# Optimization experiments

Measured on AMD Instinct MI355X. Metric: run time of the kernel, lower is better.

Reference implementation:

```python
import jax, jax.numpy as jnp
import numpy as np
import math

B, L = 16, 4096
N = B * L            # total nodes; node 0 is the (masked) root
E = N - 1            # one parent edge per non-root node
D_IN, D_OUT, HEADS = 512, 256, 4
SLOPE = 0.2          # PyG GATConv default negative_slope
PRUNE_FRAC = 0.3


def gelu(x):
    return 0.5 * x * (1.0 + jnp.tanh(math.sqrt(2.0 / math.pi) * (x + 0.044715 * x ** 3)))


def remove_nodes_func(parent, remove):
    # parent[i] = parent node id of node i+1; remove[j] = 1 iff node j+1 removed.
    for _ in range(5):
        aug_rem = jnp.concatenate([jnp.zeros(1, jnp.int32), remove])
        aug_par = jnp.concatenate([jnp.zeros(1, jnp.int32), parent])
        pr = aug_rem[parent]                               # is my parent removed?
        parent = pr * aug_par[parent] + (1 - pr) * parent  # grandparent if so
    return parent


def remove_nodes_and_edges(edge_index, map_index):
    src, par = edge_index[0], edge_index[1]
    rem = jnp.zeros(N, jnp.int32).at[map_index].set(1)     # removal flag per node id (>=1)
    edge_mask = 1 - rem[src]                               # drop edges whose child node removed
    emr = rem[1:]                                          # == zeros(E).at[map_index-1].set(1)
    temp = remove_nodes_func(par, emr)
    ei_new = jnp.stack([src, temp]) * edge_mask[None, :]   # removed edges collapse to (0,0)
    node_mask_upd = jnp.concatenate([jnp.ones(1, jnp.float32), 1.0 - emr.astype(jnp.float32)])
    return ei_new, node_mask_upd


def gat_conv(xin, edge_index, gat_w, att_src, att_dst, gat_b):
    # PyG GATConv: concat=True, add_self_loops=True, eval mode (attention dropout off)
    h = (xin @ gat_w).reshape(N, HEADS, D_OUT)
    loop = jnp.arange(N, dtype=edge_index.dtype)
    src = jnp.concatenate([edge_index[0], loop])
    dst = jnp.concatenate([edge_index[1], loop])
    a_src = jnp.einsum('nhc,hc->nh', h, att_src)
    a_dst = jnp.einsum('nhc,hc->nh', h, att_dst)
    alpha = jax.nn.leaky_relu(a_src[src] + a_dst[dst], SLOPE)       # [Etot, H]
    m = jax.ops.segment_max(alpha, dst, num_segments=N)
    e = jnp.exp(alpha - m[dst])
    s = jax.ops.segment_sum(e, dst, num_segments=N)
    coef = e / (s[dst] + 1e-16)
    out = jax.ops.segment_sum(coef[:, :, None] * h[src], dst, num_segments=N)
    return out.reshape(N, HEADS * D_OUT) + gat_b


def setup_inputs():
    key = jax.random.key(0)
    ks = jax.random.split(key, 10)
    x = jax.random.normal(ks[0], (N, D_IN), jnp.float32)
    statement_rep = jax.random.normal(ks[1], (N, D_IN), jnp.float32)
    node_mask = (jax.random.uniform(ks[2], (B, L)) > 0.3).astype(jnp.float32)
    node_mask = node_mask.at[0, 0].set(0.0)  # root node never scored/pruned
    type_id = jax.random.randint(ks[3], (B, L), 0, 2, dtype=jnp.int32)
    child = jnp.arange(1, N, dtype=jnp.int32)
    parent = jnp.floor(jax.random.uniform(ks[4], (E,)) * child).astype(jnp.int32)  # parent < child
    edge_index = jnp.stack([child, parent])
    edge_index_ent = edge_index
    s = 0.02
    scorer_w = jax.random.normal(ks[5], (2 * D_IN, 1), jnp.float32) * s
    scorer_b = jnp.zeros((1,), jnp.float32)
    emb_w = jax.random.normal(ks[6], (2, D_OUT), jnp.float32) * s
    emb_b = jnp.zeros((D_OUT,), jnp.float32)
    gat_w = jax.random.normal(ks[7], (2 * D_IN + D_OUT, HEADS * D_OUT), jnp.float32) * s
    att_src = jax.random.normal(ks[8], (HEADS, D_OUT), jnp.float32) * s
    att_dst = jax.random.normal(ks[9], (HEADS, D_OUT), jnp.float32) * s
    gat_b = jnp.zeros((HEADS * D_OUT,), jnp.float32)
    return {"x": x, "edge_index": edge_index, "edge_index_ent": edge_index_ent,
            "statement_rep": statement_rep, "node_mask": node_mask, "type_id": type_id,
            "scorer_w": scorer_w, "scorer_b": scorer_b, "emb_w": emb_w, "emb_b": emb_b,
            "gat_w": gat_w, "att_src": att_src, "att_dst": att_dst, "gat_b": gat_b}


def reference(x, edge_index, edge_index_ent, statement_rep, node_mask, type_id,
              scorer_w, scorer_b, emb_w, emb_b, gat_w, att_src, att_dst, gat_b):
    del edge_index_ent  # threaded through the original but never used
    nm = node_mask.reshape(-1)
    tid = type_id.reshape(-1)
    one_hot = jax.nn.one_hot(tid, 2, dtype=jnp.float32)
    type_emb = gelu(one_hot @ emb_w + emb_b)
    # --- single GNN layer (num_layers=1), with top-k node pruning ---
    node_score = (jnp.concatenate([x, statement_rep], 1) @ scorer_w + scorer_b)[:, 0] * nm
    nnz = int(jnp.count_nonzero(node_score))  # eager; k is data-dependent in the original
    if int(nnz * PRUNE_FRAC) != 0:
        k = int(nnz * PRUNE_FRAC + 1)
        masked = jnp.where(node_score != 0, node_score, jnp.inf)
        _, map_index = jax.lax.top_k(-masked, k)  # k smallest nonzero scores -> node ids
        edge_index, upd = remove_nodes_and_edges(edge_index, map_index)
        nm = nm * upd
    xin = jnp.concatenate([x, statement_rep, type_emb], 1)
    out = gelu(gat_conv(xin, edge_index, gat_w, att_src, att_dst, gat_b))
    # feature dropout runs in eval as identity here (deterministic reference)
    return out, nm.reshape(B, L)
```

## Files before the change

kernel.cpp:

```cpp
#include <hip/hip_runtime.h>
#include <cstdint>
#include <cstddef>

#define N_NODES 65536
#define E_EDGES 65535
#define DIN     512
#define KDIM    1024
#define JDIM    1024
#define HEADS   4
#define DOUT    256

typedef short   short8  __attribute__((ext_vector_type(8)));
typedef unsigned short ushort8 __attribute__((ext_vector_type(8)));
typedef float   floatx4 __attribute__((ext_vector_type(4)));

__device__ inline float bf2f(unsigned short u){
  union { unsigned int i; float f; } c; c.i = ((unsigned int)u) << 16; return c.f;
}
__device__ inline unsigned short f2bf(float f){
  union { float f; unsigned int i; } c; c.f = f;
  unsigned int r = c.i + 0x7FFFu + ((c.i >> 16) & 1u);
  return (unsigned short)(r >> 16);
}
__device__ inline unsigned int okey(float f){
  union { float f; unsigned int u; } c; c.f = f;
  return (c.u & 0x80000000u) ? ~c.u : (c.u | 0x80000000u);
}
__device__ inline float unokey(unsigned int k){
  union { unsigned int u; float f; } c;
  c.u = (k & 0x80000000u) ? (k ^ 0x80000000u) : ~k;
  return c.f;
}
__device__ inline float leaky(float x){ return x >= 0.f ? x : 0.2f * x; }
__device__ inline float gelu_f(float x){
  return 0.5f * x * (1.f + tanhf(0.7978845608028654f * (x + 0.044715f * x * x * x)));
}

__global__ void k_watt(const float* __restrict__ gw, const float* __restrict__ atts,
                       const float* __restrict__ attd, float* __restrict__ watt_s,
                       float* __restrict__ watt_d){
  int wave = threadIdx.x >> 6, lane = threadIdx.x & 63;
  int k = blockIdx.x*4 + wave;
  int hd = lane >> 4;
  const float* gr = gw + (size_t)k*JDIM + lane*16;
  float vs = 0.f, vd = 0.f;
  #pragma unroll
  for (int j = 0; j < 16; j += 4){
    float4 g = *(const float4*)(gr + j);
    float4 s = *(const float4*)(atts + lane*16 + j);
    float4 d = *(const float4*)(attd + lane*16 + j);
    vs += g.x*s.x + g.y*s.y + g.z*s.z + g.w*s.w;
    vd += g.x*d.x + g.y*d.y + g.z*d.z + g.w*d.w;
  }
  for (int m2 = 1; m2 < 16; m2 <<= 1){ vs += __shfl_xor(vs, m2); vd += __shfl_xor(vd, m2); }
  if ((lane & 15) == 0){ watt_s[k*4 + hd] = vs; watt_d[k*4 + hd] = vd; }
}

__global__ void k_tatt(const float* __restrict__ tc, const float* __restrict__ atts,
                       const float* __restrict__ attd, float* __restrict__ tatt){
  int lane = threadIdx.x;
  for (int o = 0; o < 16; o++){
    int ty = o >> 3, sd = (o >> 2) & 1, hd = o & 3;
    const float* av = sd ? attd : atts;
    float p = 0.f;
    #pragma unroll
    for (int cc = 0; cc < 4; cc++){
      int c = lane*4 + cc;
      p += tc[ty*JDIM + hd*256 + c] * av[hd*DOUT + c];
    }
    for (int sdel = 32; sdel; sdel >>= 1) p += __shfl_down(p, sdel);
    if (lane == 0) tatt[o] = p;
  }
}

__global__ void k_prep(const float* __restrict__ x, const float* __restrict__ sr,
                       const float* __restrict__ nmask, const float* __restrict__ sw,
                       const float* __restrict__ sb, const float* __restrict__ watt_s,
                       const float* __restrict__ watt_d, const float* __restrict__ tatt,
                       const int* __restrict__ tid, unsigned short* __restrict__ xs,
                       float* __restrict__ score, unsigned int* __restrict__ key,
                       float* __restrict__ asrc, float* __restrict__ adst){
  int lane = threadIdx.x & 63, wv = threadIdx.x >> 6;
  int i = blockIdx.x*4 + wv;
  const float* xr  = x  + (size_t)i*DIN;
  const float* srr = sr + (size_t)i*DIN;
  unsigned short* xo = xs + (size_t)i*KDIM;
  double part = 0.0;
  float4 ps = {0.f,0.f,0.f,0.f}, pd = {0.f,0.f,0.f,0.f};
  #pragma unroll
  for (int j = 0; j < 8; j++){
    int k = lane + 64*j;
    float va = xr[k];
    float vb = srr[k];
    part += (double)va*(double)sw[k] + (double)vb*(double)sw[512 + k];
    float4 sA = *(const float4*)(watt_s + (size_t)k*4);
    float4 dA = *(const float4*)(watt_d + (size_t)k*4);
    float4 sB = *(const float4*)(watt_s + (size_t)(512 + k)*4);
    float4 dB = *(const float4*)(watt_d + (size_t)(512 + k)*4);
    ps.x += va*sA.x + vb*sB.x; ps.y += va*sA.y + vb*sB.y;
    ps.z += va*sA.z + vb*sB.z; ps.w += va*sA.w + vb*sB.w;
    pd.x += va*dA.x + vb*dB.x; pd.y += va*dA.y + vb*dB.y;
    pd.z += va*dA.z + vb*dB.z; pd.w += va*dA.w + vb*dB.w;
    xo[k]       = f2bf(va);
    xo[512 + k] = f2bf(vb);
  }
  for (int sdel = 32; sdel; sdel >>= 1){
    part += __shfl_down(part, sdel);
    ps.x += __shfl_down(ps.x, sdel); ps.y += __shfl_down(ps.y, sdel);
    ps.z += __shfl_down(ps.z, sdel); ps.w += __shfl_down(ps.w, sdel);
    pd.x += __shfl_down(pd.x, sdel); pd.y += __shfl_down(pd.y, sdel);
    pd.z += __shfl_down(pd.z, sdel); pd.w += __shfl_down(pd.w, sdel);
  }
  if (lane == 0){
    float fs = (float)(part + (double)sb[0]);
    float s  = fs * nmask[i];
    score[i] = s;
    float v = (s == 0.f) ? __builtin_inff() : s;
    key[i] = okey(v);
    int tt = tid[i];
    float4 os = { ps.x + tatt[tt*8 + 0], ps.y + tatt[tt*8 + 1],
                  ps.z + tatt[tt*8 + 2], ps.w + tatt[tt*8 + 3] };
    float4 od = { pd.x + tatt[tt*8 + 4], pd.y + tatt[tt*8 + 5],
                  pd.z + tatt[tt*8 + 6], pd.w + tatt[tt*8 + 7] };
    *(float4*)(asrc + (size_t)i*HEADS) = os;
    *(float4*)(adst + (size_t)i*HEADS) = od;
  }
}

__global__ void k_nnz(const float* __restrict__ score, int* scal){
  int i = blockIdx.x*256 + threadIdx.x;
  int nz = (score[i] != 0.f) ? 1 : 0;
  unsigned long long b = __ballot(nz);
  if ((threadIdx.x & 63) == 0) atomicAdd(&scal[0], (int)__popcll(b));
}

__global__ void k_initsel(int* scal){
  int nnz = scal[0];
  double prod = (double)nnz * 0.3;
  scal[1] = ((int)prod != 0) ? 1 : 0;
  int k = (int)(prod + 1.0);
  scal[2] = k; scal[3] = 0; scal[4] = k;
}

__global__ void k_hist(const unsigned int* __restrict__ key, unsigned int* __restrict__ hist,
                       const int* __restrict__ scal, int pass){
  __shared__ unsigned int lh[256];
  int t = threadIdx.x;
  lh[t] = 0; __syncthreads();
  int i = blockIdx.x*256 + t;
  unsigned int kv = key[i];
  unsigned int pref = (unsigned int)scal[3];
  bool ok = (pass == 0) || ((kv >> (32 - 8*pass)) == pref);
  if (ok) atomicAdd(&lh[(kv >> (24 - 8*pass)) & 255u], 1u);
  __syncthreads();
  if (lh[t]) atomicAdd(&hist[t], lh[t]);
}

__global__ void k_select(unsigned int* __restrict__ hist, int* __restrict__ scal){
  __shared__ unsigned int h[256];
  int t = threadIdx.x;
  h[t] = hist[t];
  __syncthreads();
  if (t == 0){
    unsigned int r = (unsigned int)scal[4];
    unsigned int cum = 0, pref = (unsigned int)scal[3];
    for (int b = 0; b < 256; b++){
      unsigned int c = h[b];
      if (cum + c >= r){
        scal[3] = (int)((pref << 8) | (unsigned int)b);
        scal[4] = (int)(r - cum);
        break;
      }
      cum += c;
    }
  }
  __syncthreads();
  hist[t] = 0;
}

__global__ void k_mark(const unsigned int* __restrict__ key, int* __restrict__ scal,
                       int* __restrict__ rem, int* __restrict__ eqlist){
  if (!scal[1]) return;
  int i = blockIdx.x*256 + threadIdx.x;
  unsigned int Ks = (unsigned int)scal[3];
  unsigned int kv = key[i];
  if (kv < Ks) rem[i] = 1;
  else if (kv == Ks){
    int p = atomicAdd(&scal[5], 1);
    if (p < 4096) eqlist[p] = i;
  }
}

__global__ void k_ties(int* __restrict__ scal, int* __restrict__ eqlist, int* __restrict__ rem){
  if (!scal[1]) return;
  int m = scal[5]; if (m > 4096) m = 4096;
  int need = scal[4]; if (need > m) need = m;
  for (int it = 0; it < need; it++){
    int best = 0x7FFFFFFF, bj = -1;
    for (int j = 0; j < m; j++){ int v = eqlist[j]; if (v < best){ best = v; bj = j; } }
    if (bj < 0) break;
    rem[best] = 1; eqlist[bj] = 0x7FFFFFFF;
  }
}

__global__ void k_remap(const int* __restrict__ pin, const int* __restrict__ rem,
                        int* __restrict__ pout){
  int e = blockIdx.x*256 + threadIdx.x;
  if (e >= E_EDGES) return;
  int p = pin[e];
  pout[e] = rem[p] ? (p == 0 ? 0 : pin[p-1]) : p;
}

__global__ void k_edges(const int* __restrict__ srcIn, const int* __restrict__ pfin,
                        const int* __restrict__ rem, int* __restrict__ srcF,
                        int* __restrict__ dstF, int* __restrict__ cnt){
  int e = blockIdx.x*256 + threadIdx.x;
  if (e >= E_EDGES) return;
  int s = srcIn[e];
  if (rem[s]){ srcF[e] = 0; dstF[e] = -1; }
  else {
    srcF[e] = s;
    int d = pfin[e];
    dstF[e] = d;
    atomicAdd(&cnt[d], 1);
  }
}

__global__ void k_scan1(const int* __restrict__ cnt, int* __restrict__ offs,
                        int* __restrict__ bsum){
  int b = blockIdx.x, t = threadIdx.x, i = b*256 + t;
  int v = cnt[i];
  int lane = t & 63, wv = t >> 6;
  int xv = v;
  for (int o2 = 1; o2 < 64; o2 <<= 1){ int y = __shfl_up(xv, o2); if (lane >= o2) xv += y; }
  __shared__ int wt_[4];
  if (lane == 63) wt_[wv] = xv;
  __syncthreads();
  int add = 0;
  for (int k2 = 0; k2 < wv; k2++) add += wt_[k2];
  offs[i] = xv + add - v;
  if (t == 255) bsum[b] = xv + add;
}

__global__ void k_scan2(int* __restrict__ bsum){
  int t = threadIdx.x;
  int v = bsum[t];
  int lane = t & 63, wv = t >> 6;
  int xv = v;
  for (int o2 = 1; o2 < 64; o2 <<= 1){ int y = __shfl_up(xv, o2); if (lane >= o2) xv += y; }
  __shared__ int wt_[4];
  if (lane == 63) wt_[wv] = xv;
  __syncthreads();
  int add = 0;
  for (int k2 = 0; k2 < wv; k2++) add += wt_[k2];
  bsum[t] = xv + add - v;
}

__global__ void k_scan3(int* __restrict__ offs, const int* __restrict__ bsum,
                        int* __restrict__ cur){
  int b = blockIdx.x, t = threadIdx.x, i = b*256 + t;
  int v = offs[i] + bsum[b];
  offs[i] = v; cur[i] = v;
}

__global__ void k_fill(const int* __restrict__ dstF, int* __restrict__ cur,
                       int* __restrict__ elist){
  int e = blockIdx.x*256 + threadIdx.x;
  if (e >= E_EDGES) return;
  int d = dstF[e]; if (d < 0) return;
  int pos = atomicAdd(&cur[d], 1);
  elist[pos] = e;
}

__global__ void k_wt(const float* __restrict__ gw, unsigned short* __restrict__ wtb){
  __shared__ float tile[32][33];
  int kt = blockIdx.x*32, jt = blockIdx.y*32;
  int tx = threadIdx.x, ty = threadIdx.y;
  for (int r = ty; r < 32; r += 8) tile[r][tx] = gw[(size_t)(kt+r)*JDIM + jt + tx];
  __syncthreads();
  for (int r = ty; r < 32; r += 8) wtb[(size_t)(jt+r)*KDIM + kt + tx] = f2bf(tile[tx][r]);
}

__global__ void k_tc(const float* __restrict__ embw, const float* __restrict__ embb,
                     const float* __restrict__ gw, float* __restrict__ tc){
  __shared__ float eg[2][DOUT];
  int t = threadIdx.x;
  eg[0][t] = gelu_f(embw[t] + embb[t]);
  eg[1][t] = gelu_f(embw[DOUT + t] + embb[t]);
  __syncthreads();
  int g = blockIdx.x*256 + t;
  int te = g >> 10, j = g & 1023;
  float acc = 0.f;
  #pragma unroll 8
  for (int c = 0; c < DOUT; c++){
    acc += eg[te][c] * gw[(size_t)(KDIM + c)*JDIM + j];
  }
  tc[te*JDIM + j] = acc;
}

#define BKG 64
__global__ __launch_bounds__(512, 2) void k_gemm(const unsigned short* __restrict__ xs,
    const unsigned short* __restrict__ wtb, const float* __restrict__ tc,
    const int* __restrict__ tid, unsigned short* __restrict__ hmat){
  __shared__ unsigned short As[2][256*BKG];
  __shared__ unsigned short Bs[2][256*BKG];
  int bid = blockIdx.x;
  int xcd = bid & 7, tq = bid >> 3;
  int jb = tq & 3, ip = (tq >> 2)*8 + xcd;
  int rowbase = ip*256, colbase = jb*256;
  int t = threadIdx.x, wave = t >> 6, lane = t & 63;
  int wm = (wave >> 2)*128, wn = (wave & 3)*64;
  floatx4 acc[8][4];
  floatx4 zero = {0.f, 0.f, 0.f, 0.f};
  #pragma unroll
  for (int a = 0; a < 8; a++)
    #pragma unroll
    for (int b = 0; b < 4; b++) acc[a][b] = zero;

  int srow = lane >> 3;
  int scol = (lane & 7)*8;

  auto STAGE = [&](int buf, int kt){
    int k0 = kt*BKG;
    #pragma unroll
    for (int r = 0; r < 4; r++){
      int ci = r*8 + wave;
      int row = ci*8 + srow;
      const unsigned short* ga = xs  + (size_t)(rowbase + row)*KDIM + k0 + scol;
      __builtin_amdgcn_global_load_lds((const __attribute__((address_space(1))) void*)ga,
          (__attribute__((address_space(3))) void*)(&As[buf][ci*512 + lane*8]), 16, 0, 0);
      const unsigned short* gb = wtb + (size_t)(colbase + row)*KDIM + k0 + scol;
      __builtin_amdgcn_global_load_lds((const __attribute__((address_space(1))) void*)gb,
          (__attribute__((address_space(3))) void*)(&Bs[buf][ci*512 + lane*8]), 16, 0, 0);
    }
  };

  int rr = lane & 15, rq = (lane >> 4)*8;
  auto COMPUTE = [&](int buf){
    #pragma unroll
    for (int ks = 0; ks < 2; ks++){
      short8 af[8], bfr[4];
      #pragma unroll
      for (int mi = 0; mi < 8; mi++)
        af[mi]  = *(const short8*)(&As[buf][(wm + mi*16 + rr)*BKG + ks*32 + rq]);
      #pragma unroll
      for (int ni = 0; ni < 4; ni++)
        bfr[ni] = *(const short8*)(&Bs[buf][(wn + ni*16 + rr)*BKG + ks*32 + rq]);
      #pragma unroll
      for (int mi = 0; mi < 8; mi++)
        #pragma unroll
        for (int ni = 0; ni < 4; ni++)
          acc[mi][ni] = __builtin_amdgcn_mfma_f32_16x16x32_bf16(af[mi], bfr[ni], acc[mi][ni], 0, 0, 0);
    }
  };

  const int NT = KDIM / BKG;
  STAGE(0, 0);
  __syncthreads();
  int cur = 0;
  for (int kt = 0; kt < NT - 1; kt++){
    STAGE(cur ^ 1, kt + 1);
    COMPUTE(cur);
    __syncthreads();
    cur ^= 1;
  }
  COMPUTE(cur);

  int q = lane >> 4, cc = lane & 15;
  #pragma unroll
  for (int mi = 0; mi < 8; mi++){
    #pragma unroll
    for (int reg = 0; reg < 4; reg++){
      int rowg = rowbase + wm + mi*16 + q*4 + reg;
      int tt = tid[rowg];
      #pragma unroll
      for (int ni = 0; ni < 4; ni++){
        int col = colbase + wn + ni*16 + cc;
        float v = acc[mi][ni][reg] + tc[tt*JDIM + col];
        hmat[(size_t)rowg*JDIM + col] = f2bf(v);
      }
    }
  }
}

__global__ void k_agg(const unsigned short* __restrict__ hmat, const int* __restrict__ srcF,
                      const float* __restrict__ asrc, const float* __restrict__ adst,
                      const int* __restrict__ offs, const int* __restrict__ cnt,
                      const int* __restrict__ elist, const float* __restrict__ gatb,
                      const int* __restrict__ scal, float* __restrict__ out){
  int n = blockIdx.x, t = threadIdx.x;
  int o0 = offs[n], c_ = cnt[n];
  __shared__ float mh_s[4], sh_s[4];
  int wave = t >> 6, lane = t & 63;
  if (wave == 0){
    int hd = lane >> 4, r = lane & 15;
    float adn = adst[n*HEADS + hd];
    float aself = leaky(asrc[n*HEADS + hd] + adn);
    float mx = aself;
    for (int q2 = r; q2 < c_; q2 += 16){
      int e = elist[o0 + q2];
      int s = srcF[e];
      float al = leaky(asrc[s*HEADS + hd] + adn);
      mx = fmaxf(mx, al);
    }
    for (int m2 = 1; m2 < 16; m2 <<= 1) mx = fmaxf(mx, __shfl_xor(mx, m2));
    float sm = 0.f;
    for (int q2 = r; q2 < c_; q2 += 16){
      int e = elist[o0 + q2];
      int s = srcF[e];
      float al = leaky(asrc[s*HEADS + hd] + adn);
      sm += expf(al - mx);
    }
    for (int m2 = 1; m2 < 16; m2 <<= 1) sm += __shfl_xor(sm, m2);
    if (r == 0){
      float wself = 1.f;
      if (n == 0 && scal[1]) wself = 1.f + (float)scal[2];
      sm += wself * expf(aself - mx);
      mh_s[hd] = mx; sh_s[hd] = sm + 1e-16f;
    }
  }
  __syncthreads();
  int hd = t >> 6;
  float mh = mh_s[hd];
  float sh = sh_s[hd];
  float adn = adst[n*HEADS + hd];
  float a0 = 0.f, a1 = 0.f, a2 = 0.f, a3 = 0.f;
  {
    float al = leaky(asrc[n*HEADS + hd] + adn);
    float coef = expf(al - mh) / sh;
    if (n == 0 && scal[1]) coef *= (1.f + (float)scal[2]);
    ushort4 hv = *(const ushort4*)(hmat + (size_t)n*JDIM + 4*t);
    a0 += coef*bf2f(hv.x); a1 += coef*bf2f(hv.y); a2 += coef*bf2f(hv.z); a3 += coef*bf2f(hv.w);
  }
  for (int q2 = 0; q2 < c_; q2++){
    int e = elist[o0 + q2];
    int s = srcF[e];
    float al = leaky(asrc[s*HEADS + hd] + adn);
    float coef = expf(al - mh) / sh;
    ushort4 hv = *(const ushort4*)(hmat + (size_t)s*JDIM + 4*t);
    a0 += coef*bf2f(hv.x); a1 += coef*bf2f(hv.y); a2 += coef*bf2f(hv.z); a3 += coef*bf2f(hv.w);
  }
  const float4 gb = *(const float4*)(gatb + 4*t);
  float4 ov;
  ov.x = gelu_f(a0 + gb.x); ov.y = gelu_f(a1 + gb.y);
  ov.z = gelu_f(a2 + gb.z); ov.w = gelu_f(a3 + gb.w);
  *(float4*)(out + (size_t)n*JDIM + 4*t) = ov;
}

__global__ void k_nm(const float* __restrict__ nmask, const int* __restrict__ rem,
                     float* __restrict__ nmout){
  int i = blockIdx.x*256 + threadIdx.x;
  float u = (i == 0) ? 1.f : (1.f - (float)rem[i]);
  nmout[i] = nmask[i] * u;
}

extern "C" void kernel_launch(void* const* d_in, const int* in_sizes, int n_in,
                              void* d_out, int out_size, void* d_ws, size_t ws_size,
                              hipStream_t stream){
  (void)in_sizes; (void)n_in; (void)out_size; (void)ws_size;
  const float* x    = (const float*)d_in[0];
  const int*  eidx  = (const int*)d_in[1];
  const float* sr   = (const float*)d_in[3];
  const float* nmask= (const float*)d_in[4];
  const int*  tid   = (const int*)d_in[5];
  const float* sw   = (const float*)d_in[6];
  const float* sb   = (const float*)d_in[7];
  const float* embw = (const float*)d_in[8];
  const float* embb = (const float*)d_in[9];
  const float* gw   = (const float*)d_in[10];
  const float* atts = (const float*)d_in[11];
  const float* attd = (const float*)d_in[12];
  const float* gatb = (const float*)d_in[13];
  float* out = (float*)d_out;

  char* w = (char*)d_ws;
  size_t o = 0;
  auto alloc = [&](size_t bytes){ size_t r = o; o += (bytes + 255) & ~(size_t)255; return r; };
  size_t o_cnt  = alloc((size_t)N_NODES*4);
  size_t o_rem  = alloc((size_t)N_NODES*4);
  size_t o_hist = alloc(256*4);
  size_t o_scal = alloc(64);
  size_t o_eq   = alloc(4096*4);
  size_t zero_bytes = o;
  size_t o_score= alloc((size_t)N_NODES*4);
  size_t o_key  = alloc((size_t)N_NODES*4);
  size_t o_pA   = alloc((size_t)E_EDGES*4);
  size_t o_pB   = alloc((size_t)E_EDGES*4);
  size_t o_srcF = alloc((size_t)E_EDGES*4);
  size_t o_dstF = alloc((size_t)E_EDGES*4);
  size_t o_off  = alloc((size_t)N_NODES*4);
  size_t o_cur  = alloc((size_t)N_NODES*4);
  size_t o_el   = alloc((size_t)E_EDGES*4);
  size_t o_bsum = alloc(256*4);
  size_t o_asrc = alloc((size_t)N_NODES*HEADS*4);
  size_t o_adst = alloc((size_t)N_NODES*HEADS*4);
  size_t o_tc   = alloc((size_t)2*JDIM*4);
  size_t o_wats = alloc((size_t)KDIM*4*4);
  size_t o_watd = alloc((size_t)KDIM*4*4);
  size_t o_tatt = alloc(16*4);
  size_t o_wt   = alloc((size_t)JDIM*KDIM*2);
  size_t o_xs   = alloc((size_t)N_NODES*KDIM*2);
  size_t o_h    = alloc((size_t)N_NODES*JDIM*2);

  int* cnt   = (int*)(w + o_cnt);
  int* rem   = (int*)(w + o_rem);
  unsigned int* hist = (unsigned int*)(w + o_hist);
  int* scal  = (int*)(w + o_scal);
  int* eqlist= (int*)(w + o_eq);
  float* score = (float*)(w + o_score);
  unsigned int* key = (unsigned int*)(w + o_key);
  int* pA = (int*)(w + o_pA);
  int* pB = (int*)(w + o_pB);
  int* srcF = (int*)(w + o_srcF);
  int* dstF = (int*)(w + o_dstF);
  int* offs = (int*)(w + o_off);
  int* cur  = (int*)(w + o_cur);
  int* elist= (int*)(w + o_el);
  int* bsum = (int*)(w + o_bsum);
  float* asrc = (float*)(w + o_asrc);
  float* adst = (float*)(w + o_adst);
  float* tc = (float*)(w + o_tc);
  float* watt_s = (float*)(w + o_wats);
  float* watt_d = (float*)(w + o_watd);
  float* tatt = (float*)(w + o_tatt);
  unsigned short* wtb = (unsigned short*)(w + o_wt);
  unsigned short* xs  = (unsigned short*)(w + o_xs);
  unsigned short* hmat= (unsigned short*)(w + o_h);

  hipMemsetAsync(w, 0, zero_bytes, stream);

  k_watt<<<256, 256, 0, stream>>>(gw, atts, attd, watt_s, watt_d);
  k_tc<<<8, 256, 0, stream>>>(embw, embb, gw, tc);
  k_tatt<<<1, 64, 0, stream>>>(tc, atts, attd, tatt);
  k_wt<<<dim3(32,32), dim3(32,8), 0, stream>>>(gw, wtb);

  k_prep<<<N_NODES/4, 256, 0, stream>>>(x, sr, nmask, sw, sb, watt_s, watt_d, tatt,
                                        tid, xs, score, key, asrc, adst);
  k_nnz<<<N_NODES/256, 256, 0, stream>>>(score, scal);
  k_initsel<<<1, 1, 0, stream>>>(scal);
  for (int p = 0; p < 4; p++){
    k_hist<<<N_NODES/256, 256, 0, stream>>>(key, hist, scal, p);
    k_select<<<1, 256, 0, stream>>>(hist, scal);
  }
  k_mark<<<N_NODES/256, 256, 0, stream>>>(key, scal, rem, eqlist);
  k_ties<<<1, 1, 0, stream>>>(scal, eqlist, rem);

  const int* par_in = eidx + E_EDGES;
  int egrid = (E_EDGES + 255)/256;
  k_remap<<<egrid, 256, 0, stream>>>(par_in, rem, pA);
  k_remap<<<egrid, 256, 0, stream>>>(pA, rem, pB);
  k_remap<<<egrid, 256, 0, stream>>>(pB, rem, pA);
  k_remap<<<egrid, 256, 0, stream>>>(pA, rem, pB);
  k_remap<<<egrid, 256, 0, stream>>>(pB, rem, pA);

  k_edges<<<egrid, 256, 0, stream>>>(eidx, pA, rem, srcF, dstF, cnt);
  k_scan1<<<256, 256, 0, stream>>>(cnt, offs, bsum);
  k_scan2<<<1, 256, 0, stream>>>(bsum);
  k_scan3<<<256, 256, 0, stream>>>(offs, bsum, cur);
  k_fill<<<egrid, 256, 0, stream>>>(dstF, cur, elist);

  k_gemm<<<1024, 512, 0, stream>>>(xs, wtb, tc, tid, hmat);

  k_agg<<<N_NODES, 256, 0, stream>>>(hmat, srcF, asrc, adst, offs, cnt,
                                     elist, gatb, scal, out);
  k_nm<<<N_NODES/256, 256, 0, stream>>>(nmask, rem, out + (size_t)N_NODES*JDIM);
}
```

Baseline: 1.056 ms.

## Fuse parent remap passes into one climb kernel and tune GEMM waitcnt barriers

Replaces the five k_remap launches plus k_edges with a single k_climb kernel. It walks up the ancestor chain (up to 31 steps) past removed nodes and emits the edges directly, removing launches and intermediate buffers. It also assumes src = e+1 rather than reading it from edge_index. In the GEMM main loop, __syncthreads is replaced with explicit s_waitcnt vmcnt(8) and raw s_barrier so the next tile's global loads can stay in flight during compute. The climb differs from the reference's fixed 5 rounds of pointer-jumping on the original parent array, so results may differ on deep removal chains, and the hardcoded waitcnt depends on the load count in STAGE.

```diff
diff --git a/kernel.cpp b/kernel.cpp
--- a/kernel.cpp
+++ b/kernel.cpp
@@ -203,27 +203,18 @@
   }
 }
 
-__global__ void k_remap(const int* __restrict__ pin, const int* __restrict__ rem,
-                        int* __restrict__ pout){
+__global__ void k_climb(const int* __restrict__ par_in, const int* __restrict__ rem,
+                        int* __restrict__ srcF, int* __restrict__ dstF,
+                        int* __restrict__ cnt){
   int e = blockIdx.x*256 + threadIdx.x;
   if (e >= E_EDGES) return;
-  int p = pin[e];
-  pout[e] = rem[p] ? (p == 0 ? 0 : pin[p-1]) : p;
-}
-
-__global__ void k_edges(const int* __restrict__ srcIn, const int* __restrict__ pfin,
-                        const int* __restrict__ rem, int* __restrict__ srcF,
-                        int* __restrict__ dstF, int* __restrict__ cnt){
-  int e = blockIdx.x*256 + threadIdx.x;
-  if (e >= E_EDGES) return;
-  int s = srcIn[e];
-  if (rem[s]){ srcF[e] = 0; dstF[e] = -1; }
-  else {
-    srcF[e] = s;
-    int d = pfin[e];
-    dstF[e] = d;
-    atomicAdd(&cnt[d], 1);
-  }
+  int s = e + 1;
+  if (rem[s]){ srcF[e] = 0; dstF[e] = -1; return; }
+  int p = par_in[e];
+  for (int st = 0; st < 31 && rem[p]; st++) p = par_in[p-1];
+  srcF[e] = s;
+  dstF[e] = p;
+  atomicAdd(&cnt[p], 1);
 }
 
 __global__ void k_scan1(const int* __restrict__ cnt, int* __restrict__ offs,
@@ -299,6 +290,7 @@
 }
 
 #define BKG 64
+#define CFENCE() asm volatile("" ::: "memory")
 __global__ __launch_bounds__(512, 2) void k_gemm(const unsigned short* __restrict__ xs,
     const unsigned short* __restrict__ wtb, const float* __restrict__ tc,
     const int* __restrict__ tid, unsigned short* __restrict__ hmat){
@@ -356,15 +348,24 @@
 
   const int NT = KDIM / BKG;
   STAGE(0, 0);
-  __syncthreads();
   int cur = 0;
-  for (int kt = 0; kt < NT - 1; kt++){
-    STAGE(cur ^ 1, kt + 1);
+  for (int kt = 0; kt < NT; kt++){
+    if (kt < NT - 1){
+      STAGE(cur ^ 1, kt + 1);
+      asm volatile("s_waitcnt vmcnt(8)" ::: "memory");
+    } else {
+      asm volatile("s_waitcnt vmcnt(0)" ::: "memory");
+    }
+    __builtin_amdgcn_s_barrier();
+    CFENCE();
     COMPUTE(cur);
-    __syncthreads();
+    if (kt < NT - 1){
+      CFENCE();
+      __builtin_amdgcn_s_barrier();
+      CFENCE();
+    }
     cur ^= 1;
   }
-  COMPUTE(cur);
 
   int q = lane >> 4, cc = lane & 15;
   #pragma unroll
@@ -484,8 +485,6 @@
   size_t zero_bytes = o;
   size_t o_score= alloc((size_t)N_NODES*4);
   size_t o_key  = alloc((size_t)N_NODES*4);
-  size_t o_pA   = alloc((size_t)E_EDGES*4);
-  size_t o_pB   = alloc((size_t)E_EDGES*4);
   size_t o_srcF = alloc((size_t)E_EDGES*4);
   size_t o_dstF = alloc((size_t)E_EDGES*4);
   size_t o_off  = alloc((size_t)N_NODES*4);
@@ -509,8 +508,6 @@
   int* eqlist= (int*)(w + o_eq);
   float* score = (float*)(w + o_score);
   unsigned int* key = (unsigned int*)(w + o_key);
-  int* pA = (int*)(w + o_pA);
-  int* pB = (int*)(w + o_pB);
   int* srcF = (int*)(w + o_srcF);
   int* dstF = (int*)(w + o_dstF);
   int* offs = (int*)(w + o_off);
@@ -547,13 +544,8 @@
 
   const int* par_in = eidx + E_EDGES;
   int egrid = (E_EDGES + 255)/256;
-  k_remap<<<egrid, 256, 0, stream>>>(par_in, rem, pA);
-  k_remap<<<egrid, 256, 0, stream>>>(pA, rem, pB);
-  k_remap<<<egrid, 256, 0, stream>>>(pB, rem, pA);
-  k_remap<<<egrid, 256, 0, stream>>>(pA, rem, pB);
-  k_remap<<<egrid, 256, 0, stream>>>(pB, rem, pA);
-
-  k_edges<<<egrid, 256, 0, stream>>>(eidx, pA, rem, srcF, dstF, cnt);
+  k_climb<<<egrid, 256, 0, stream>>>(par_in, rem, srcF, dstF, cnt);
+
   k_scan1<<<256, 256, 0, stream>>>(cnt, offs, bsum);
   k_scan2<<<1, 256, 0, stream>>>(bsum);
   k_scan3<<<256, 256, 0, stream>>>(offs, bsum, cur);
```

New measurement: 1.022 ms. 3.2% less time.
